# Kernel optimization log

Measured on AMD Instinct MI355X. Metric: run time of the kernel, lower is better.

Reference implementation:

```python
import jax, jax.numpy as jnp
import numpy as np

N_QUBITS = 4
LAYERS = 1

# state has shape [N] + [2]*n; qubit w lives on axis w+1 (wire 0 = most significant, as in PennyLane)

def _apply_ry(state, theta, w, n):
    s0 = jnp.take(state, 0, axis=w + 1)
    s1 = jnp.take(state, 1, axis=w + 1)
    shp = (-1,) + (1,) * (n - 1)
    c = jnp.cos(theta / 2).reshape(shp)
    s = jnp.sin(theta / 2).reshape(shp)
    return jnp.stack([c * s0 - s * s1, s * s0 + c * s1], axis=w + 1)


def _apply_crx(state, theta, ctrl, tgt, n):
    sub0 = jnp.take(state, 0, axis=ctrl + 1)  # control = 0 subspace (unchanged)
    sub1 = jnp.take(state, 1, axis=ctrl + 1)  # control = 1 subspace -> RX on target
    t_ax = tgt + 1 if tgt < ctrl else tgt     # target axis inside sub1 ([N] at axis 0)
    a0 = jnp.take(sub1, 0, axis=t_ax)
    a1 = jnp.take(sub1, 1, axis=t_ax)
    shp = (-1,) + (1,) * (n - 2)
    c = jnp.cos(theta / 2).reshape(shp).astype(state.dtype)
    s = jnp.sin(theta / 2).reshape(shp).astype(state.dtype)
    new1 = jnp.stack([c * a0 - 1j * s * a1, -1j * s * a0 + c * a1], axis=t_ax)
    return jnp.stack([sub0, new1], axis=ctrl + 1)


def run_circuit(params):
    """Ansatz 14 (arXiv:1905.10876) applied to |0...0>, batched over tokens. params: [N, 4*n*layers]."""
    n = N_QUBITS
    N = params.shape[0]
    state = jnp.zeros((N,) + (2,) * n, jnp.complex64)
    state = state.at[(slice(None),) + (0,) * n].set(1.0)
    idx = 0
    for _ in range(LAYERS):
        for i in range(n):
            state = _apply_ry(state, params[:, idx], i, n); idx += 1
        for i in range(n - 1, -1, -1):
            state = _apply_crx(state, params[:, idx], i, (i + 1) % n, n); idx += 1
        for i in range(n):
            state = _apply_ry(state, params[:, idx], i, n); idx += 1
        for i in [n - 1] + list(range(n - 1)):
            state = _apply_crx(state, params[:, idx], i, (i - 1) % n, n); idx += 1
    return state


def measure_xyz(state, n):
    """<X_w>, <Y_w>, <Z_w> for all wires; order matches the PennyLane qnode (all X, all Y, all Z)."""
    N = state.shape[0]
    xs, ys, zs = [], [], []
    for w in range(n):
        s0 = jnp.take(state, 0, axis=w + 1).reshape(N, -1)
        s1 = jnp.take(state, 1, axis=w + 1).reshape(N, -1)
        prod = jnp.sum(jnp.conj(s0) * s1, axis=-1)
        xs.append(2.0 * jnp.real(prod))
        ys.append(2.0 * jnp.imag(prod))
        zs.append(jnp.sum(jnp.abs(s0) ** 2 - jnp.abs(s1) ** 2, axis=-1))
    return jnp.stack(xs + ys + zs, axis=-1)  # [N, 3n]


def setup_inputs() -> dict:
    key = jax.random.key(0)
    k = jax.random.split(key, 7)
    B, L, S, H, E = 2, 2048, 2048, 8, 64
    n_params = 4 * N_QUBITS * LAYERS  # 16
    queries = jax.random.normal(k[0], (B, L, H, E), jnp.float32)
    keys = jax.random.normal(k[1], (B, S, H, E), jnp.float32)
    values = jax.random.normal(k[2], (B, S, H, E), jnp.float32)
    W_angles = jax.random.normal(k[3], (n_params, E), jnp.float32) * 0.125   # Linear(d_model -> 16)
    b_angles = jax.random.normal(k[4], (n_params,), jnp.float32) * 0.125
    W_out = jax.random.normal(k[5], (E, 3 * N_QUBITS), jnp.float32) * 0.28   # Linear(12 -> d_model)
    b_out = jax.random.normal(k[6], (E,), jnp.float32) * 0.28
    return {"queries": queries, "keys": keys, "values": values,
            "W_angles": W_angles, "b_angles": b_angles, "W_out": W_out, "b_out": b_out}


def reference(queries, keys, values, W_angles, b_angles, W_out, b_out):
    B, L, H, E = queries.shape
    S = keys.shape[1]
    scale = 1.0 / np.sqrt(E)
    # quantum encoding of values: angles -> PQC from |0> -> X/Y/Z expvals -> linear map to d_model
    angles = jnp.einsum('bshd,pd->bshp', values, W_angles) + b_angles      # [B,S,H,16]
    state = run_circuit(angles.reshape(-1, angles.shape[-1]))              # [N, 2,2,2,2]
    meas = measure_xyz(state, N_QUBITS)                                    # [N, 12]
    qev = (meas @ W_out.T + b_out).reshape(B, S, H, E)                     # [B,S,H,D]
    # classical attention (eval mode: dropout = identity)
    scores = jnp.einsum('blhe,bshe->bhls', queries, keys)
    mask = jnp.triu(jnp.ones((L, S), bool), 1)
    scores = jnp.where(mask[None, None], -1e9, scores)
    A = jax.nn.softmax(scale * scores, axis=-1)
    return jnp.einsum('bhls,bshd->blhd', A, qev)
```

## Files before the change

### kernel.cpp

```cpp
#include <hip/hip_runtime.h>

#define NP   16
#define EDIM 64
#define HH   8
#define BB   2
#define LL   2048
#define SS   2048
#define NQT  32
#define LDP  72

typedef __attribute__((ext_vector_type(8))) short bf16x8;
typedef __attribute__((ext_vector_type(4))) float f32x4;

__device__ __forceinline__ float bf2f(unsigned int u) {
    union { unsigned int i; float f; } x; x.i = u << 16; return x.f;
}
__device__ __forceinline__ unsigned short f2bf(float f) {
    union { float ff; unsigned int i; } x; x.ff = f;
    unsigned int r = x.i + 0x7fffu + ((x.i >> 16) & 1u);
    return (unsigned short)(r >> 16);
}
__device__ __forceinline__ unsigned int pk2(float a, float b) {
    return (unsigned int)f2bf(a) | ((unsigned int)f2bf(b) << 16);
}
__device__ __forceinline__ unsigned int tpk2(float a, float b) {
    union { float f; unsigned int i; } xa, xb; xa.f = a; xb.f = b;
    return (xa.i >> 16) | (xb.i & 0xffff0000u);
}

__device__ __forceinline__ void stage16s(const float* __restrict__ g, unsigned short* l, float sc) {
    const float4* gp = (const float4*)g;
    float4 v0 = gp[0], v1 = gp[1], v2 = gp[2], v3 = gp[3];
    uint4 w0, w1;
    w0.x = pk2(v0.x * sc, v0.y * sc); w0.y = pk2(v0.z * sc, v0.w * sc);
    w0.z = pk2(v1.x * sc, v1.y * sc); w0.w = pk2(v1.z * sc, v1.w * sc);
    w1.x = pk2(v2.x * sc, v2.y * sc); w1.y = pk2(v2.z * sc, v2.w * sc);
    w1.z = pk2(v3.x * sc, v3.y * sc); w1.w = pk2(v3.z * sc, v3.w * sc);
    ((uint4*)l)[0] = w0; ((uint4*)l)[1] = w1;
}

#define INV4PI 0.07957747154594767f

__global__ __launch_bounds__(64)
void qev6_kernel(const float* __restrict__ values,
                 const float* __restrict__ key,
                 const float* __restrict__ Wang, const float* __restrict__ bang,
                 const float* __restrict__ Wout, const float* __restrict__ bout,
                 unsigned short* __restrict__ qevb,
                 unsigned short* __restrict__ Kb)
{
    const int tid = threadIdx.x;
    const int bx  = blockIdx.x;
    const int h   = blockIdx.y;
    const int b   = blockIdx.z;

    if (bx >= 32) {
        const int s0 = (bx - 32) * 64;
        const float* ks = key + ((size_t)b * SS * HH + h) * EDIM;
        unsigned short* kd = Kb + ((size_t)(b * HH + h) * SS + s0) * EDIM;
        float4 v[16];
#pragma unroll
        for (int i = 0; i < 16; i++) {
            const int u = i * 64 + tid;
            const int row = u >> 4, ch = u & 15;
            v[i] = *(const float4*)(ks + (size_t)(s0 + row) * HH * EDIM + ch * 4);
        }
#pragma unroll
        for (int i = 0; i < 16; i++) {
            const int u = i * 64 + tid;
            const int row = u >> 4, ch = u & 15;
            uint2 w2; w2.x = pk2(v[i].x, v[i].y); w2.y = pk2(v[i].z, v[i].w);
            *(uint2*)&kd[row * EDIM + ch * 4] = w2;
        }
        return;
    }

    __shared__ float sW[NP * EDIM];
    __shared__ float sWo[EDIM * 12];
    __shared__ float sba[NP];
    __shared__ float sbo[EDIM];

    const int s0 = bx * 64;

#pragma unroll
    for (int i = 0; i < 4; i++) ((float4*)sW)[i * 64 + tid] = ((const float4*)Wang)[i * 64 + tid];
#pragma unroll
    for (int i = 0; i < 3; i++) ((float4*)sWo)[i * 64 + tid] = ((const float4*)Wout)[i * 64 + tid];
    if (tid < NP) sba[tid] = bang[tid];
    sbo[tid] = bout[tid];
    __syncthreads();

    const float* vptr = values + ((size_t)(b * SS + s0 + tid) * HH + h) * EDIM;
    float4 vv[16];
#pragma unroll
    for (int c = 0; c < 16; c++) vv[c] = ((const float4*)vptr)[c];

    float ang[NP];
#pragma unroll
    for (int p = 0; p < NP; p++) ang[p] = sba[p];
#pragma unroll
    for (int c = 0; c < 16; c++) {
#pragma unroll
        for (int p = 0; p < NP; p++) {
            float a = ang[p];
            a = fmaf(sW[p * EDIM + c * 4 + 0], vv[c].x, a);
            a = fmaf(sW[p * EDIM + c * 4 + 1], vv[c].y, a);
            a = fmaf(sW[p * EDIM + c * 4 + 2], vv[c].z, a);
            a = fmaf(sW[p * EDIM + c * 4 + 3], vv[c].w, a);
            ang[p] = a;
        }
    }

    float sc[NP], cc[NP];
#pragma unroll
    for (int p = 0; p < NP; p++) {
        float u = ang[p] * INV4PI;
        sc[p] = __builtin_amdgcn_sinf(u);
        cc[p] = __builtin_amdgcn_cosf(u);
    }

    float sr[16], si[16];
#pragma unroll
    for (int i = 0; i < 16; i++) { sr[i] = 0.f; si[i] = 0.f; }
    sr[0] = 1.f;

    auto RY = [&](int w, float s, float c) {
        const int bit = 8 >> w;
#pragma unroll
        for (int i = 0; i < 16; i++) {
            if (!(i & bit)) {
                const int j = i | bit;
                float a0r = sr[i], a0i = si[i], a1r = sr[j], a1i = si[j];
                sr[i] = c * a0r - s * a1r;  si[i] = c * a0i - s * a1i;
                sr[j] = s * a0r + c * a1r;  si[j] = s * a0i + c * a1i;
            }
        }
    };
    auto CRX = [&](int cw, int tw, float s, float c) {
        const int cbit = 8 >> cw, tbit = 8 >> tw;
#pragma unroll
        for (int i = 0; i < 16; i++) {
            if ((i & cbit) && !(i & tbit)) {
                const int j = i | tbit;
                float a0r = sr[i], a0i = si[i], a1r = sr[j], a1i = si[j];
                sr[i] =  c * a0r + s * a1i;  si[i] =  c * a0i - s * a1r;
                sr[j] =  s * a0i + c * a1r;  si[j] = -s * a0r + c * a1i;
            }
        }
    };

    RY(0, sc[0], cc[0]); RY(1, sc[1], cc[1]); RY(2, sc[2], cc[2]); RY(3, sc[3], cc[3]);
    CRX(3, 0, sc[4], cc[4]); CRX(2, 3, sc[5], cc[5]); CRX(1, 2, sc[6], cc[6]); CRX(0, 1, sc[7], cc[7]);
    RY(0, sc[8], cc[8]); RY(1, sc[9], cc[9]); RY(2, sc[10], cc[10]); RY(3, sc[11], cc[11]);
    CRX(3, 2, sc[12], cc[12]); CRX(0, 3, sc[13], cc[13]); CRX(1, 0, sc[14], cc[14]); CRX(2, 1, sc[15], cc[15]);

    float meas[12];
#pragma unroll
    for (int w = 0; w < 4; w++) {
        const int bit = 8 >> w;
        float pr = 0.f, pi = 0.f, z = 0.f;
#pragma unroll
        for (int i = 0; i < 16; i++) {
            if (!(i & bit)) {
                const int j = i | bit;
                pr += sr[i] * sr[j] + si[i] * si[j];
                pi += sr[i] * si[j] - si[i] * sr[j];
                z  += sr[i] * sr[i] + si[i] * si[i] - sr[j] * sr[j] - si[j] * si[j];
            }
        }
        meas[w] = 2.f * pr; meas[4 + w] = 2.f * pi; meas[8 + w] = z;
    }

    unsigned short* ob = qevb + ((size_t)(b * HH + h) * EDIM) * SS + s0 + tid;
#pragma unroll
    for (int eb = 0; eb < 4; eb++) {
        float acc[16];
#pragma unroll
        for (int j = 0; j < 16; j++) acc[j] = sbo[eb * 16 + j];
#pragma unroll
        for (int mm = 0; mm < 12; mm++)
#pragma unroll
            for (int j = 0; j < 16; j++)
                acc[j] = fmaf(meas[mm], sWo[(eb * 16 + j) * 12 + mm], acc[j]);
#pragma unroll
        for (int j = 0; j < 16; j++)
            ob[(size_t)(eb * 16 + j) * SS] = f2bf(acc[j]);
    }
}

__global__ __launch_bounds__(256, 2)
void attn7_kernel(const float* __restrict__ qry,
                  const unsigned short* __restrict__ Kb,
                  const unsigned short* __restrict__ Vb,
                  float* __restrict__ out)
{
    __shared__ unsigned short Qs[64 * LDP];
    __shared__ unsigned short Pq[4][64 * LDP];
    __shared__ float Lbuf[16 * 64];

    const int tid  = threadIdx.x;
    const int id   = blockIdx.x;
    const int hf2  = id >> 8;
    const int r    = id & 255;
    const int qt   = hf2 ? (NQT - 1 - (r >> 4)) : (r >> 4);
    const int hb   = r & 15;
    const int h    = hb & 7;
    const int b    = hb >> 3;

    const int w    = tid >> 6;
    const int lane = tid & 63;
    const int ml   = lane & 15;
    const int quad = lane >> 4;
    const int srow = tid >> 2;
    const int sch  = tid & 3;

    const unsigned short* kbase = Kb + (size_t)(b * HH + h) * SS * EDIM;
    const unsigned short* vbase = Vb + (size_t)(b * HH + h) * EDIM * SS;
    unsigned short* Pw = &Pq[w][0];

    const int q0 = qt * 64;

    stage16s(qry + (((size_t)b * LL + q0 + srow) * HH + h) * EDIM + sch * 16,
             &Qs[srow * LDP + sch * 16], 0.125f);
    __syncthreads();

    bf16x8 bq[4][2];
#pragma unroll
    for (int ntq = 0; ntq < 4; ntq++) {
        bq[ntq][0] = *(const bf16x8*)&Qs[(16 * ntq + ml) * LDP + quad * 8];
        bq[ntq][1] = *(const bf16x8*)&Qs[(16 * ntq + ml) * LDP + quad * 8 + 32];
    }

    f32x4 oaccT[4][4];
    float lacc[4] = {0.f, 0.f, 0.f, 0.f};
#pragma unroll
    for (int i = 0; i < 4; i++)
#pragma unroll
        for (int j = 0; j < 4; j++) oaccT[i][j] = (f32x4)(0.f);

    int t = w;
    uint4 kc[8];
    if (t <= qt) {
#pragma unroll
        for (int f = 0; f < 8; f++) {
            const int mt = f >> 1, hf = f & 1;
            kc[f] = *(const uint4*)(kbase + (size_t)(t * 64 + 16 * mt + ml) * EDIM + quad * 8 + 32 * hf);
        }
    }

    for (; t <= qt; t += 4) {
        const bool diag = (t == qt);
        const bool more = (t + 4 <= qt);

        uint4 vc[8];
#pragma unroll
        for (int f = 0; f < 8; f++) {
            const int mt = f >> 1, hf = f & 1;
            vc[f] = *(const uint4*)(vbase + (size_t)(16 * mt + ml) * SS + t * 64 + quad * 8 + 32 * hf);
        }
        uint4 kn[8];
        if (more) {
#pragma unroll
            for (int f = 0; f < 8; f++) {
                const int mt = f >> 1, hf = f & 1;
                kn[f] = *(const uint4*)(kbase + (size_t)((t + 4) * 64 + 16 * mt + ml) * EDIM + quad * 8 + 32 * hf);
            }
        }

#pragma unroll
        for (int mts = 0; mts < 4; mts++)
#pragma unroll
            for (int ntq = 0; ntq < 4; ntq++) {
                f32x4 s = __builtin_amdgcn_mfma_f32_16x16x32_bf16(
                    *(const bf16x8*)&kc[2 * mts], bq[ntq][0], (f32x4)(0.f), 0, 0, 0);
                s = __builtin_amdgcn_mfma_f32_16x16x32_bf16(
                    *(const bf16x8*)&kc[2 * mts + 1], bq[ntq][1], s, 0, 0, 0);
                float p0 = __expf(s[0]), p1 = __expf(s[1]), p2 = __expf(s[2]), p3 = __expf(s[3]);
                if (diag) {
                    const int sbase = 16 * mts + 4 * quad, qcol = 16 * ntq + ml;
                    if (sbase + 0 > qcol) p0 = 0.f;
                    if (sbase + 1 > qcol) p1 = 0.f;
                    if (sbase + 2 > qcol) p2 = 0.f;
                    if (sbase + 3 > qcol) p3 = 0.f;
                }
                lacc[ntq] += (p0 + p1) + (p2 + p3);
                uint2 u; u.x = tpk2(p0, p1); u.y = tpk2(p2, p3);
                *(uint2*)&Pw[(16 * ntq + ml) * LDP + 16 * mts + 4 * quad] = u;
            }

#pragma unroll
        for (int ntq = 0; ntq < 4; ntq++) {
            bf16x8 pb0 = *(const bf16x8*)&Pw[(16 * ntq + ml) * LDP + quad * 8];
            bf16x8 pb1 = *(const bf16x8*)&Pw[(16 * ntq + ml) * LDP + quad * 8 + 32];
#pragma unroll
            for (int mte = 0; mte < 4; mte++) {
                oaccT[mte][ntq] = __builtin_amdgcn_mfma_f32_16x16x32_bf16(
                    *(const bf16x8*)&vc[2 * mte], pb0, oaccT[mte][ntq], 0, 0, 0);
                oaccT[mte][ntq] = __builtin_amdgcn_mfma_f32_16x16x32_bf16(
                    *(const bf16x8*)&vc[2 * mte + 1], pb1, oaccT[mte][ntq], 0, 0, 0);
            }
        }

        if (more) {
#pragma unroll
            for (int f = 0; f < 8; f++) kc[f] = kn[f];
        }
    }

#pragma unroll
    for (int mte = 0; mte < 4; mte++)
#pragma unroll
        for (int ntq = 0; ntq < 4; ntq++) {
            uint2 u;
            u.x = pk2(oaccT[mte][ntq][0], oaccT[mte][ntq][1]);
            u.y = pk2(oaccT[mte][ntq][2], oaccT[mte][ntq][3]);
            *(uint2*)&Pw[(16 * ntq + ml) * LDP + 16 * mte + 4 * quad] = u;
        }
#pragma unroll
    for (int ntq = 0; ntq < 4; ntq++)
        Lbuf[(w * 4 + quad) * 64 + 16 * ntq + ml] = lacc[ntq];

    __syncthreads();

    {
        const int q = tid >> 2, c = tid & 3;
        float lsum = 0.f;
#pragma unroll
        for (int i = 0; i < 16; i++) lsum += Lbuf[i * 64 + q];
        const float inv = 1.f / lsum;
        float* orow = out + (((size_t)b * LL + q0 + q) * HH + h) * EDIM;
#pragma unroll
        for (int c4 = 0; c4 < 4; c4++) {
            const int e0 = c * 16 + c4 * 4;
            float a0 = 0.f, a1 = 0.f, a2 = 0.f, a3 = 0.f;
#pragma unroll
            for (int wv = 0; wv < 4; wv++) {
                uint2 u = *(const uint2*)&Pq[wv][q * LDP + e0];
                a0 += bf2f(u.x & 0xffffu); a1 += bf2f(u.x >> 16);
                a2 += bf2f(u.y & 0xffffu); a3 += bf2f(u.y >> 16);
            }
            float4 r; r.x = a0 * inv; r.y = a1 * inv; r.z = a2 * inv; r.w = a3 * inv;
            *(float4*)&orow[e0] = r;
        }
    }
}

extern "C" void kernel_launch(void* const* d_in, const int* in_sizes, int n_in,
                              void* d_out, int out_size, void* d_ws, size_t ws_size,
                              hipStream_t stream)
{
    const float* qry  = (const float*)d_in[0];
    const float* key  = (const float*)d_in[1];
    const float* val  = (const float*)d_in[2];
    const float* Wang = (const float*)d_in[3];
    const float* bang = (const float*)d_in[4];
    const float* Wout = (const float*)d_in[5];
    const float* bout = (const float*)d_in[6];
    float* out = (float*)d_out;

    const size_t seg = (size_t)BB * HH * EDIM * SS * 2;
    unsigned short* qevb = (unsigned short*)d_ws;
    unsigned short* Kb   = (unsigned short*)((char*)d_ws + seg);

    (void)in_sizes; (void)n_in; (void)out_size; (void)ws_size;

    qev6_kernel<<<dim3(64, HH, BB), 64, 0, stream>>>(val, key, Wang, bang, Wout, bout, qevb, Kb);
    attn7_kernel<<<dim3(512, 1, 1), 256, 0, stream>>>(qry, Kb, qevb, out);
}
```

Measured before the change: 113.0 us.

## Fuse QEV/key-convert prologue into attention kernel with a software grid barrier

Merges the quantum value-encoding and key bf16 conversion kernel into the attention kernel. Each block does one 64-row chunk, with wave 0 computing the circuit and wave 1 converting keys, then all blocks meet at a global atomic barrier before attention. This removes a kernel launch and the gap between the two kernels. It also adds s_setprio around the softmax and PV MFMA sections. The barrier needs all 512 blocks to be resident at once (256 CUs x 2), or it deadlocks, and two waves per block sit idle during the prologue.

```diff
diff --git a/kernel.cpp b/kernel.cpp
--- a/kernel.cpp
+++ b/kernel.cpp
@@ -41,181 +41,190 @@
 
 #define INV4PI 0.07957747154594767f
 
-__global__ __launch_bounds__(64)
-void qev6_kernel(const float* __restrict__ values,
-                 const float* __restrict__ key,
-                 const float* __restrict__ Wang, const float* __restrict__ bang,
-                 const float* __restrict__ Wout, const float* __restrict__ bout,
-                 unsigned short* __restrict__ qevb,
-                 unsigned short* __restrict__ Kb)
+__device__ unsigned int g_cnt   = 0;
+__device__ unsigned int g_phase = 0;
+
+__global__ __launch_bounds__(256, 2)
+void fused_kernel(const float* __restrict__ qry,
+                  const float* __restrict__ key,
+                  const float* __restrict__ values,
+                  const float* __restrict__ Wang, const float* __restrict__ bang,
+                  const float* __restrict__ Wout, const float* __restrict__ bout,
+                  unsigned short* __restrict__ qevb,
+                  unsigned short* __restrict__ Kb,
+                  float* __restrict__ out)
 {
-    const int tid = threadIdx.x;
-    const int bx  = blockIdx.x;
-    const int h   = blockIdx.y;
-    const int b   = blockIdx.z;
-
-    if (bx >= 32) {
-        const int s0 = (bx - 32) * 64;
-        const float* ks = key + ((size_t)b * SS * HH + h) * EDIM;
-        unsigned short* kd = Kb + ((size_t)(b * HH + h) * SS + s0) * EDIM;
-        float4 v[16];
-#pragma unroll
-        for (int i = 0; i < 16; i++) {
-            const int u = i * 64 + tid;
-            const int row = u >> 4, ch = u & 15;
-            v[i] = *(const float4*)(ks + (size_t)(s0 + row) * HH * EDIM + ch * 4);
-        }
-#pragma unroll
-        for (int i = 0; i < 16; i++) {
-            const int u = i * 64 + tid;
-            const int row = u >> 4, ch = u & 15;
-            uint2 w2; w2.x = pk2(v[i].x, v[i].y); w2.y = pk2(v[i].z, v[i].w);
-            *(uint2*)&kd[row * EDIM + ch * 4] = w2;
-        }
-        return;
-    }
-
     __shared__ float sW[NP * EDIM];
     __shared__ float sWo[EDIM * 12];
     __shared__ float sba[NP];
     __shared__ float sbo[EDIM];
-
-    const int s0 = bx * 64;
-
-#pragma unroll
-    for (int i = 0; i < 4; i++) ((float4*)sW)[i * 64 + tid] = ((const float4*)Wang)[i * 64 + tid];
-#pragma unroll
-    for (int i = 0; i < 3; i++) ((float4*)sWo)[i * 64 + tid] = ((const float4*)Wout)[i * 64 + tid];
-    if (tid < NP) sba[tid] = bang[tid];
-    sbo[tid] = bout[tid];
-    __syncthreads();
-
-    const float* vptr = values + ((size_t)(b * SS + s0 + tid) * HH + h) * EDIM;
-    float4 vv[16];
-#pragma unroll
-    for (int c = 0; c < 16; c++) vv[c] = ((const float4*)vptr)[c];
-
-    float ang[NP];
-#pragma unroll
-    for (int p = 0; p < NP; p++) ang[p] = sba[p];
-#pragma unroll
-    for (int c = 0; c < 16; c++) {
-#pragma unroll
-        for (int p = 0; p < NP; p++) {
-            float a = ang[p];
-            a = fmaf(sW[p * EDIM + c * 4 + 0], vv[c].x, a);
-            a = fmaf(sW[p * EDIM + c * 4 + 1], vv[c].y, a);
-            a = fmaf(sW[p * EDIM + c * 4 + 2], vv[c].z, a);
-            a = fmaf(sW[p * EDIM + c * 4 + 3], vv[c].w, a);
-            ang[p] = a;
-        }
-    }
-
-    float sc[NP], cc[NP];
-#pragma unroll
-    for (int p = 0; p < NP; p++) {
-        float u = ang[p] * INV4PI;
-        sc[p] = __builtin_amdgcn_sinf(u);
-        cc[p] = __builtin_amdgcn_cosf(u);
-    }
-
-    float sr[16], si[16];
-#pragma unroll
-    for (int i = 0; i < 16; i++) { sr[i] = 0.f; si[i] = 0.f; }
-    sr[0] = 1.f;
-
-    auto RY = [&](int w, float s, float c) {
-        const int bit = 8 >> w;
-#pragma unroll
-        for (int i = 0; i < 16; i++) {
-            if (!(i & bit)) {
-                const int j = i | bit;
-                float a0r = sr[i], a0i = si[i], a1r = sr[j], a1i = si[j];
-                sr[i] = c * a0r - s * a1r;  si[i] = c * a0i - s * a1i;
-                sr[j] = s * a0r + c * a1r;  si[j] = s * a0i + c * a1i;
-            }
-        }
-    };
-    auto CRX = [&](int cw, int tw, float s, float c) {
-        const int cbit = 8 >> cw, tbit = 8 >> tw;
-#pragma unroll
-        for (int i = 0; i < 16; i++) {
-            if ((i & cbit) && !(i & tbit)) {
-                const int j = i | tbit;
-                float a0r = sr[i], a0i = si[i], a1r = sr[j], a1i = si[j];
-                sr[i] =  c * a0r + s * a1i;  si[i] =  c * a0i - s * a1r;
-                sr[j] =  s * a0i + c * a1r;  si[j] = -s * a0r + c * a1i;
-            }
-        }
-    };
-
-    RY(0, sc[0], cc[0]); RY(1, sc[1], cc[1]); RY(2, sc[2], cc[2]); RY(3, sc[3], cc[3]);
-    CRX(3, 0, sc[4], cc[4]); CRX(2, 3, sc[5], cc[5]); CRX(1, 2, sc[6], cc[6]); CRX(0, 1, sc[7], cc[7]);
-    RY(0, sc[8], cc[8]); RY(1, sc[9], cc[9]); RY(2, sc[10], cc[10]); RY(3, sc[11], cc[11]);
-    CRX(3, 2, sc[12], cc[12]); CRX(0, 3, sc[13], cc[13]); CRX(1, 0, sc[14], cc[14]); CRX(2, 1, sc[15], cc[15]);
-
-    float meas[12];
-#pragma unroll
-    for (int w = 0; w < 4; w++) {
-        const int bit = 8 >> w;
-        float pr = 0.f, pi = 0.f, z = 0.f;
-#pragma unroll
-        for (int i = 0; i < 16; i++) {
-            if (!(i & bit)) {
-                const int j = i | bit;
-                pr += sr[i] * sr[j] + si[i] * si[j];
-                pi += sr[i] * si[j] - si[i] * sr[j];
-                z  += sr[i] * sr[i] + si[i] * si[i] - sr[j] * sr[j] - si[j] * si[j];
-            }
-        }
-        meas[w] = 2.f * pr; meas[4 + w] = 2.f * pi; meas[8 + w] = z;
-    }
-
-    unsigned short* ob = qevb + ((size_t)(b * HH + h) * EDIM) * SS + s0 + tid;
-#pragma unroll
-    for (int eb = 0; eb < 4; eb++) {
-        float acc[16];
-#pragma unroll
-        for (int j = 0; j < 16; j++) acc[j] = sbo[eb * 16 + j];
-#pragma unroll
-        for (int mm = 0; mm < 12; mm++)
-#pragma unroll
-            for (int j = 0; j < 16; j++)
-                acc[j] = fmaf(meas[mm], sWo[(eb * 16 + j) * 12 + mm], acc[j]);
-#pragma unroll
-        for (int j = 0; j < 16; j++)
-            ob[(size_t)(eb * 16 + j) * SS] = f2bf(acc[j]);
-    }
-}
-
-__global__ __launch_bounds__(256, 2)
-void attn7_kernel(const float* __restrict__ qry,
-                  const unsigned short* __restrict__ Kb,
-                  const unsigned short* __restrict__ Vb,
-                  float* __restrict__ out)
-{
     __shared__ unsigned short Qs[64 * LDP];
     __shared__ unsigned short Pq[4][64 * LDP];
     __shared__ float Lbuf[16 * 64];
 
     const int tid  = threadIdx.x;
     const int id   = blockIdx.x;
-    const int hf2  = id >> 8;
-    const int r    = id & 255;
-    const int qt   = hf2 ? (NQT - 1 - (r >> 4)) : (r >> 4);
-    const int hb   = r & 15;
-    const int h    = hb & 7;
-    const int b    = hb >> 3;
-
     const int w    = tid >> 6;
     const int lane = tid & 63;
+
+    ((float4*)sW)[tid & 255] = ((const float4*)Wang)[tid & 255];
+    if (tid < 192) ((float4*)sWo)[tid] = ((const float4*)Wout)[tid];
+    if (tid < NP) sba[tid] = bang[tid];
+    if (tid < 64) sbo[tid] = bout[tid];
+    __syncthreads();
+
+    const int chunk = id >> 4;
+    const int hb1   = id & 15;
+    const int h1    = hb1 & 7;
+    const int b1    = hb1 >> 3;
+    const int s0p   = chunk * 64;
+
+    if (w == 0) {
+        const float* vptr = values + ((size_t)(b1 * SS + s0p + lane) * HH + h1) * EDIM;
+        float4 vv[16];
+#pragma unroll
+        for (int c = 0; c < 16; c++) vv[c] = ((const float4*)vptr)[c];
+
+        float ang[NP];
+#pragma unroll
+        for (int p = 0; p < NP; p++) ang[p] = sba[p];
+#pragma unroll
+        for (int c = 0; c < 16; c++) {
+#pragma unroll
+            for (int p = 0; p < NP; p++) {
+                float a = ang[p];
+                a = fmaf(sW[p * EDIM + c * 4 + 0], vv[c].x, a);
+                a = fmaf(sW[p * EDIM + c * 4 + 1], vv[c].y, a);
+                a = fmaf(sW[p * EDIM + c * 4 + 2], vv[c].z, a);
+                a = fmaf(sW[p * EDIM + c * 4 + 3], vv[c].w, a);
+                ang[p] = a;
+            }
+        }
+
+        float sc[NP], cc[NP];
+#pragma unroll
+        for (int p = 0; p < NP; p++) {
+            float u = ang[p] * INV4PI;
+            sc[p] = __builtin_amdgcn_sinf(u);
+            cc[p] = __builtin_amdgcn_cosf(u);
+        }
+
+        float sr[16], si[16];
+#pragma unroll
+        for (int i = 0; i < 16; i++) { sr[i] = 0.f; si[i] = 0.f; }
+        sr[0] = 1.f;
+
+        auto RY = [&](int wq, float s, float c) {
+            const int bit = 8 >> wq;
+#pragma unroll
+            for (int i = 0; i < 16; i++) {
+                if (!(i & bit)) {
+                    const int j = i | bit;
+                    float a0r = sr[i], a0i = si[i], a1r = sr[j], a1i = si[j];
+                    sr[i] = c * a0r - s * a1r;  si[i] = c * a0i - s * a1i;
+                    sr[j] = s * a0r + c * a1r;  si[j] = s * a0i + c * a1i;
+                }
+            }
+        };
+        auto CRX = [&](int cw, int tw, float s, float c) {
+            const int cbit = 8 >> cw, tbit = 8 >> tw;
+#pragma unroll
+            for (int i = 0; i < 16; i++) {
+                if ((i & cbit) && !(i & tbit)) {
+                    const int j = i | tbit;
+                    float a0r = sr[i], a0i = si[i], a1r = sr[j], a1i = si[j];
+                    sr[i] =  c * a0r + s * a1i;  si[i] =  c * a0i - s * a1r;
+                    sr[j] =  s * a0i + c * a1r;  si[j] = -s * a0r + c * a1i;
+                }
+            }
+        };
+
+        RY(0, sc[0], cc[0]); RY(1, sc[1], cc[1]); RY(2, sc[2], cc[2]); RY(3, sc[3], cc[3]);
+        CRX(3, 0, sc[4], cc[4]); CRX(2, 3, sc[5], cc[5]); CRX(1, 2, sc[6], cc[6]); CRX(0, 1, sc[7], cc[7]);
+        RY(0, sc[8], cc[8]); RY(1, sc[9], cc[9]); RY(2, sc[10], cc[10]); RY(3, sc[11], cc[11]);
+        CRX(3, 2, sc[12], cc[12]); CRX(0, 3, sc[13], cc[13]); CRX(1, 0, sc[14], cc[14]); CRX(2, 1, sc[15], cc[15]);
+
+        float meas[12];
+#pragma unroll
+        for (int wq = 0; wq < 4; wq++) {
+            const int bit = 8 >> wq;
+            float pr = 0.f, pi = 0.f, z = 0.f;
+#pragma unroll
+            for (int i = 0; i < 16; i++) {
+                if (!(i & bit)) {
+                    const int j = i | bit;
+                    pr += sr[i] * sr[j] + si[i] * si[j];
+                    pi += sr[i] * si[j] - si[i] * sr[j];
+                    z  += sr[i] * sr[i] + si[i] * si[i] - sr[j] * sr[j] - si[j] * si[j];
+                }
+            }
+            meas[wq] = 2.f * pr; meas[4 + wq] = 2.f * pi; meas[8 + wq] = z;
+        }
+
+        unsigned short* ob = qevb + ((size_t)(b1 * HH + h1) * EDIM) * SS + s0p + lane;
+#pragma unroll
+        for (int eb = 0; eb < 4; eb++) {
+            float acc[16];
+#pragma unroll
+            for (int j = 0; j < 16; j++) acc[j] = sbo[eb * 16 + j];
+#pragma unroll
+            for (int mm = 0; mm < 12; mm++)
+#pragma unroll
+                for (int j = 0; j < 16; j++)
+                    acc[j] = fmaf(meas[mm], sWo[(eb * 16 + j) * 12 + mm], acc[j]);
+#pragma unroll
+            for (int j = 0; j < 16; j++)
+                ob[(size_t)(eb * 16 + j) * SS] = f2bf(acc[j]);
+        }
+    } else if (w == 1) {
+        const float* ks = key + ((size_t)b1 * SS * HH + h1) * EDIM;
+        unsigned short* kd = Kb + ((size_t)(b1 * HH + h1) * SS + s0p) * EDIM;
+        float4 v[16];
+#pragma unroll
+        for (int i = 0; i < 16; i++) {
+            const int u = i * 64 + lane;
+            const int row = u >> 4, ch = u & 15;
+            v[i] = *(const float4*)(ks + (size_t)(s0p + row) * HH * EDIM + ch * 4);
+        }
+#pragma unroll
+        for (int i = 0; i < 16; i++) {
+            const int u = i * 64 + lane;
+            const int row = u >> 4, ch = u & 15;
+            uint2 w2; w2.x = pk2(v[i].x, v[i].y); w2.y = pk2(v[i].z, v[i].w);
+            *(uint2*)&kd[row * EDIM + ch * 4] = w2;
+        }
+    }
+
+    __threadfence();
+    __syncthreads();
+    if (tid == 0) {
+        const unsigned int ph = __hip_atomic_load(&g_phase, __ATOMIC_ACQUIRE, __HIP_MEMORY_SCOPE_AGENT);
+        const unsigned int old = __hip_atomic_fetch_add(&g_cnt, 1u, __ATOMIC_ACQ_REL, __HIP_MEMORY_SCOPE_AGENT);
+        if (old == (unsigned int)(gridDim.x - 1)) {
+            __hip_atomic_store(&g_cnt, 0u, __ATOMIC_RELAXED, __HIP_MEMORY_SCOPE_AGENT);
+            __hip_atomic_fetch_add(&g_phase, 1u, __ATOMIC_RELEASE, __HIP_MEMORY_SCOPE_AGENT);
+        } else {
+            while (__hip_atomic_load(&g_phase, __ATOMIC_ACQUIRE, __HIP_MEMORY_SCOPE_AGENT) == ph)
+                __builtin_amdgcn_s_sleep(8);
+        }
+    }
+    __syncthreads();
+    __threadfence();
+
+    const int hf2 = id >> 8;
+    const int r   = id & 255;
+    const int qt  = hf2 ? (NQT - 1 - (r >> 4)) : (r >> 4);
+    const int hb  = r & 15;
+    const int h   = hb & 7;
+    const int b   = hb >> 3;
+
     const int ml   = lane & 15;
     const int quad = lane >> 4;
     const int srow = tid >> 2;
     const int sch  = tid & 3;
 
     const unsigned short* kbase = Kb + (size_t)(b * HH + h) * SS * EDIM;
-    const unsigned short* vbase = Vb + (size_t)(b * HH + h) * EDIM * SS;
+    const unsigned short* vbase = qevb + (size_t)(b * HH + h) * EDIM * SS;
     unsigned short* Pw = &Pq[w][0];
 
     const int q0 = qt * 64;
@@ -267,6 +276,7 @@
             }
         }
 
+        __builtin_amdgcn_s_setprio(1);
 #pragma unroll
         for (int mts = 0; mts < 4; mts++)
 #pragma unroll
@@ -287,7 +297,9 @@
                 uint2 u; u.x = tpk2(p0, p1); u.y = tpk2(p2, p3);
                 *(uint2*)&Pw[(16 * ntq + ml) * LDP + 16 * mts + 4 * quad] = u;
             }
-
+        __builtin_amdgcn_s_setprio(0);
+
+        __builtin_amdgcn_s_setprio(1);
 #pragma unroll
         for (int ntq = 0; ntq < 4; ntq++) {
             bf16x8 pb0 = *(const bf16x8*)&Pw[(16 * ntq + ml) * LDP + quad * 8];
@@ -300,6 +312,7 @@
                     *(const bf16x8*)&vc[2 * mte + 1], pb1, oaccT[mte][ntq], 0, 0, 0);
             }
         }
+        __builtin_amdgcn_s_setprio(0);
 
         if (more) {
 #pragma unroll
@@ -339,8 +352,8 @@
                 a0 += bf2f(u.x & 0xffffu); a1 += bf2f(u.x >> 16);
                 a2 += bf2f(u.y & 0xffffu); a3 += bf2f(u.y >> 16);
             }
-            float4 r; r.x = a0 * inv; r.y = a1 * inv; r.z = a2 * inv; r.w = a3 * inv;
-            *(float4*)&orow[e0] = r;
+            float4 r4; r4.x = a0 * inv; r4.y = a1 * inv; r4.z = a2 * inv; r4.w = a3 * inv;
+            *(float4*)&orow[e0] = r4;
         }
     }
 }
@@ -364,6 +377,6 @@
 
     (void)in_sizes; (void)n_in; (void)out_size; (void)ws_size;
 
-    qev6_kernel<<<dim3(64, HH, BB), 64, 0, stream>>>(val, key, Wang, bang, Wout, bout, qevb, Kb);
-    attn7_kernel<<<dim3(512, 1, 1), 256, 0, stream>>>(qry, Kb, qevb, out);
-}
+    fused_kernel<<<dim3(512, 1, 1), 256, 0, stream>>>(
+        qry, key, val, Wang, bang, Wout, bout, qevb, Kb, out);
+}
```

Result: slower. 252.3 us (+123.2%).
